# Performance work log

Measured on AMD Instinct MI355X. Metric: run time of the kernel, lower is better.

## Reference

```python
import jax, jax.numpy as jnp
import numpy as np

B, N, E = 4096, 64, 256      # graph pairs, nodes per drug, directed edges per drug
F, H, FP = 128, 64, 2048     # node feat dim, hidden dim, fingerprint dim


def setup_inputs() -> dict:
    key = jax.random.key(0)
    ks = jax.random.split(key, 14)
    return {
        "x1": jax.random.normal(ks[0], (B, N, F), jnp.float32),
        "x2": jax.random.normal(ks[1], (B, N, F), jnp.float32),
        "edge1": jax.random.randint(ks[2], (B, 2, E), 0, N, jnp.int32),
        "edge2": jax.random.randint(ks[3], (B, 2, E), 0, N, jnp.int32),
        "fp1": jax.random.uniform(ks[4], (B, FP), jnp.float32),
        "fp2": jax.random.uniform(ks[5], (B, FP), jnp.float32),
        "W1": jax.random.normal(ks[6], (F, H), jnp.float32) * 0.05,
        "b1": jnp.zeros((H,), jnp.float32),
        "W2": jax.random.normal(ks[7], (H, H), jnp.float32) * 0.05,
        "b2": jnp.zeros((H,), jnp.float32),
        "Wm1": jax.random.normal(ks[8], (2 * H + 2 * FP, 256), jnp.float32) * 0.02,
        "bm1": jnp.zeros((256,), jnp.float32),
        "Wm2": jax.random.normal(ks[9], (256, 1), jnp.float32) * 0.05,
        "bm2": jnp.zeros((1,), jnp.float32),
    }


def gcn_conv(x, src, dst, W, b):
    """PyG GCNConv: self-loops + symmetric normalization, aggregated at dst."""
    n = x.shape[0]
    loops = jnp.arange(n, dtype=src.dtype)
    s = jnp.concatenate([src, loops])
    d = jnp.concatenate([dst, loops])
    deg = jax.ops.segment_sum(jnp.ones_like(d, jnp.float32), d, num_segments=n)
    norm = jax.lax.rsqrt(deg)                      # deg >= 1 due to self-loops
    xw = x @ W                                     # [n, H]
    msg = xw[s] * (norm[s] * norm[d])[:, None]     # [n+E, H]
    return jax.ops.segment_sum(msg, d, num_segments=n) + b


def encode(x, edges, W1, b1, W2, b2):
    src, dst = edges[0], edges[1]
    h = jax.nn.relu(gcn_conv(x, src, dst, W1, b1))
    h = jax.nn.relu(gcn_conv(h, src, dst, W2, b2))
    return h.mean(axis=0)                          # global_mean_pool (1 graph)


_encode_b = jax.vmap(encode, in_axes=(0, 0, None, None, None, None))


def reference(x1, x2, edge1, edge2, fp1, fp2, W1, b1, W2, b2, Wm1, bm1, Wm2, bm2):
    h1 = _encode_b(x1, edge1, W1, b1, W2, b2)      # [B, H]
    h2 = _encode_b(x2, edge2, W1, b1, W2, b2)      # [B, H]
    fused = jnp.concatenate([h1, h2, fp1, fp2], axis=1)  # [B, 2H+2FP]
    hidden = jax.nn.relu(fused @ Wm1 + bm1)
    return jax.nn.sigmoid(hidden @ Wm2 + bm2).reshape(-1)
```

## Files before the change

kernel.cpp:

```cpp
#include <hip/hip_runtime.h>
#include <math.h>

#define B_PAIRS 4096
#define NNODES  64
#define NEDGES  256
#define FDIM    128
#define HDIM    64
#define FPDIM   2048
#define MDIM    256
#define KTOT    4224

typedef __attribute__((ext_vector_type(4))) float f32x4;
typedef __bf16 bf16x8 __attribute__((ext_vector_type(8)));

__device__ __forceinline__ unsigned short f2bf(float f) {
    return __builtin_bit_cast(unsigned short, (__bf16)f);
}
__device__ __forceinline__ unsigned pack2(float a, float b) {
    return (unsigned)f2bf(a) | ((unsigned)f2bf(b) << 16);
}
__device__ __forceinline__ unsigned long long pack4(float a, float b, float c, float d) {
    return (unsigned long long)pack2(a, b) | ((unsigned long long)pack2(c, d) << 32);
}

__global__ void prep_weights(const float* __restrict__ W1, const float* __restrict__ W2,
                             unsigned short* __restrict__ W1t, unsigned short* __restrict__ W2t) {
    const int t0 = blockIdx.x * 256 + threadIdx.x;
    const int stride = gridDim.x * 256;
    for (int i = t0; i < HDIM * FDIM; i += stride) {
        const int n = i >> 7, k = i & 127;
        W1t[i] = f2bf(W1[k * HDIM + n]);
    }
    for (int i = t0; i < HDIM * HDIM; i += stride) {
        const int n = i >> 6, k = i & 63;
        W2t[i] = f2bf(W2[k * HDIM + n]);
    }
}

__global__ __launch_bounds__(256)
void prep_wm1(const float* __restrict__ Wm1, unsigned short* __restrict__ Wm1t) {
    __shared__ float tile[32][33];
    const int k0 = blockIdx.x * 32, n0 = blockIdx.y * 32;
    const int t = threadIdx.x;
    const int c = t & 31, r8 = t >> 5;
    #pragma unroll
    for (int rr = r8; rr < 32; rr += 8)
        tile[rr][c] = Wm1[(size_t)(k0 + rr) * MDIM + n0 + c];
    __syncthreads();
    #pragma unroll
    for (int j = 0; j < 4; ++j) {
        const int n = n0 + r8 + 8 * j;
        Wm1t[(size_t)n * KTOT + k0 + c] = f2bf(tile[c][r8 + 8 * j]);
    }
}

#define WAITLDS() do { __asm__ volatile("s_waitcnt lgkmcnt(0)" ::: "memory"); \
                       __builtin_amdgcn_sched_barrier(0); } while (0)

__global__ __launch_bounds__(64, 2)
void encode_kernel(const float* __restrict__ x1, const float* __restrict__ x2,
                   const int* __restrict__ e1, const int* __restrict__ e2,
                   const unsigned short* __restrict__ W1t, const float* __restrict__ b1,
                   const unsigned short* __restrict__ W2t, const float* __restrict__ b2,
                   float* __restrict__ hbuf) {
    __shared__ __align__(16) unsigned char lds[8960];
    const int gid  = blockIdx.x;
    const int drug = gid >> 12;
    const int b    = gid & (B_PAIRS - 1);
    const float* x  = (drug ? x2 : x1) + (size_t)b * NNODES * FDIM;
    const int*   eg = (drug ? e2 : e1) + (size_t)b * 2 * NEDGES;

    const int t  = threadIdx.x;
    const int lr = t & 15, lg = t >> 4;
    const unsigned swl = (unsigned)(lr & 7) << 4;

    unsigned* cnt = (unsigned*)lds;
    float*    nrm = (float*)(lds + 8448);
    int*      deg = (int*)(lds + 8704);

    float4 xalo[16];
    #pragma unroll
    for (int mt = 0; mt < 2; ++mt) {
        const float* xr = x + (size_t)(16 * mt + lr) * FDIM + 8 * lg;
        #pragma unroll
        for (int ks = 0; ks < 4; ++ks) {
            xalo[mt * 8 + 2 * ks]     = ((const float4*)(xr + 32 * ks))[0];
            xalo[mt * 8 + 2 * ks + 1] = ((const float4*)(xr + 32 * ks))[1];
        }
    }
    const int4 s4 = ((const int4*)eg)[t];
    const int4 d4 = ((const int4*)eg)[t + 64];

    #pragma unroll
    for (int i = 0; i < 8; ++i) ((uint4*)cnt)[t + 64 * i] = make_uint4(0, 0, 0, 0);
    if (t < 16) ((uint4*)cnt)[512 + t] = make_uint4(0, 0, 0, 0);
    deg[t] = 0;
    WAITLDS();

    {
        const int ss[4] = {s4.x, s4.y, s4.z, s4.w};
        const int dd[4] = {d4.x, d4.y, d4.z, d4.w};
        #pragma unroll
        for (int i = 0; i < 4; ++i) {
            atomicAdd(&deg[dd[i]], 1);
            atomicAdd(&cnt[dd[i] * 33 + (ss[i] >> 1)], 1u << ((ss[i] & 1) * 16));
        }
    }
    WAITLDS();

    float4 xahi[16];
    #pragma unroll
    for (int mt = 0; mt < 2; ++mt) {
        const float* xr2 = x + (size_t)(16 * (mt + 2) + lr) * FDIM + 8 * lg;
        #pragma unroll
        for (int ks = 0; ks < 4; ++ks) {
            xahi[mt * 8 + 2 * ks]     = ((const float4*)(xr2 + 32 * ks))[0];
            xahi[mt * 8 + 2 * ks + 1] = ((const float4*)(xr2 + 32 * ks))[1];
        }
    }

    nrm[t] = rsqrtf((float)deg[t] + 1.0f);
    WAITLDS();

    bf16x8 bw1[16];
    #pragma unroll
    for (int nt = 0; nt < 4; ++nt)
        #pragma unroll
        for (int ks = 0; ks < 4; ++ks)
            bw1[nt * 4 + ks] = *(const bf16x8*)(W1t + (16 * nt + lr) * FDIM + 32 * ks + 8 * lg);

    bf16x8 ahat[8];
    {
        const float ncol[2][8] = {
            { nrm[8 * lg + 0], nrm[8 * lg + 1], nrm[8 * lg + 2], nrm[8 * lg + 3],
              nrm[8 * lg + 4], nrm[8 * lg + 5], nrm[8 * lg + 6], nrm[8 * lg + 7] },
            { nrm[32 + 8 * lg + 0], nrm[32 + 8 * lg + 1], nrm[32 + 8 * lg + 2], nrm[32 + 8 * lg + 3],
              nrm[32 + 8 * lg + 4], nrm[32 + 8 * lg + 5], nrm[32 + 8 * lg + 6], nrm[32 + 8 * lg + 7] }
        };
        #pragma unroll
        for (int q = 0; q < 4; ++q) {
            const int r = 16 * q + lr;
            const float nr = nrm[r];
            #pragma unroll
            for (int ks = 0; ks < 2; ++ks) {
                const int c0 = 32 * ks + 8 * lg;
                const uint4 w = *(const uint4*)(cnt + r * 33 + (c0 >> 1));
                const unsigned ww[4] = { w.x, w.y, w.z, w.w };
                bf16x8 f;
                #pragma unroll
                for (int e = 0; e < 8; ++e) {
                    const int c = c0 + e;
                    const unsigned m = (e & 1) ? (ww[e >> 1] >> 16) : (ww[e >> 1] & 0xffffu);
                    const float v = (float)(m + (r == c ? 1u : 0u)) * nr * ncol[ks][e];
                    f[e] = (__bf16)v;
                }
                ahat[q * 2 + ks] = f;
            }
        }
    }
    WAITLDS();

    #pragma unroll
    for (int half = 0; half < 2; ++half) {
        const float4* xs = half ? xahi : xalo;
        #pragma unroll
        for (int m2i = 0; m2i < 2; ++m2i) {
            const int mt = half * 2 + m2i;
            f32x4 acc[4];
            #pragma unroll
            for (int nt = 0; nt < 4; ++nt) acc[nt] = (f32x4){0.f, 0.f, 0.f, 0.f};
            #pragma unroll
            for (int ks = 0; ks < 4; ++ks) {
                bf16x8 a;
                const float4 u = xs[m2i * 8 + 2 * ks], v = xs[m2i * 8 + 2 * ks + 1];
                a[0] = (__bf16)u.x; a[1] = (__bf16)u.y; a[2] = (__bf16)u.z; a[3] = (__bf16)u.w;
                a[4] = (__bf16)v.x; a[5] = (__bf16)v.y; a[6] = (__bf16)v.z; a[7] = (__bf16)v.w;
                #pragma unroll
                for (int nt = 0; nt < 4; ++nt)
                    acc[nt] = __builtin_amdgcn_mfma_f32_16x16x32_bf16(a, bw1[nt * 4 + ks], acc[nt], 0, 0, 0);
            }
            const unsigned m2 = (unsigned)(2 * (16 * mt + 4 * lg));
            #pragma unroll
            for (int nt = 0; nt < 4; ++nt) {
                const int f = 16 * nt + lr;
                *(unsigned long long*)(lds + (unsigned)f * 128 + (m2 ^ swl)) =
                    pack4(acc[nt][0], acc[nt][1], acc[nt][2], acc[nt][3]);
            }
        }
    }
    WAITLDS();

    {
        bf16x8 ta[8];
        #pragma unroll
        for (int mt = 0; mt < 4; ++mt)
            #pragma unroll
            for (int ks = 0; ks < 2; ++ks)
                ta[mt * 2 + ks] = *(const bf16x8*)(lds + (unsigned)(16 * mt + lr) * 128 +
                                                   (((unsigned)(64 * ks + 16 * lg)) ^ swl));
        WAITLDS();
        #pragma unroll
        for (int mt = 0; mt < 4; ++mt) {
            f32x4 acc[4];
            #pragma unroll
            for (int nt = 0; nt < 4; ++nt) acc[nt] = (f32x4){0.f, 0.f, 0.f, 0.f};
            #pragma unroll
            for (int ks = 0; ks < 2; ++ks)
                #pragma unroll
                for (int nt = 0; nt < 4; ++nt)
                    acc[nt] = __builtin_amdgcn_mfma_f32_16x16x32_bf16(ta[mt * 2 + ks], ahat[nt * 2 + ks], acc[nt], 0, 0, 0);
            const int m0 = 16 * mt + 4 * lg;
            const float4 b1v = *(const float4*)(b1 + m0);
            const unsigned m2 = (unsigned)(2 * m0);
            #pragma unroll
            for (int nt = 0; nt < 4; ++nt) {
                const int d = 16 * nt + lr;
                const float v0 = fmaxf(acc[nt][0] + b1v.x, 0.f);
                const float v1 = fmaxf(acc[nt][1] + b1v.y, 0.f);
                const float v2 = fmaxf(acc[nt][2] + b1v.z, 0.f);
                const float v3 = fmaxf(acc[nt][3] + b1v.w, 0.f);
                *(unsigned long long*)(lds + (unsigned)d * 128 + (m2 ^ swl)) =
                    pack4(v0, v1, v2, v3);
            }
        }
    }
    WAITLDS();

    {
        bf16x8 ta[8], bw2[8];
        #pragma unroll
        for (int mt = 0; mt < 4; ++mt)
            #pragma unroll
            for (int ks = 0; ks < 2; ++ks)
                ta[mt * 2 + ks] = *(const bf16x8*)(lds + (unsigned)(16 * mt + lr) * 128 +
                                                   (((unsigned)(64 * ks + 16 * lg)) ^ swl));
        #pragma unroll
        for (int nt = 0; nt < 4; ++nt)
            #pragma unroll
            for (int ks = 0; ks < 2; ++ks)
                bw2[nt * 2 + ks] = *(const bf16x8*)(W2t + (16 * nt + lr) * HDIM + 32 * ks + 8 * lg);
        WAITLDS();
        #pragma unroll
        for (int mt = 0; mt < 4; ++mt) {
            f32x4 acc[4];
            #pragma unroll
            for (int nt = 0; nt < 4; ++nt) acc[nt] = (f32x4){0.f, 0.f, 0.f, 0.f};
            #pragma unroll
            for (int ks = 0; ks < 2; ++ks)
                #pragma unroll
                for (int nt = 0; nt < 4; ++nt)
                    acc[nt] = __builtin_amdgcn_mfma_f32_16x16x32_bf16(ta[mt * 2 + ks], bw2[nt * 2 + ks], acc[nt], 0, 0, 0);
            const unsigned m2 = (unsigned)(2 * (16 * mt + 4 * lg));
            #pragma unroll
            for (int nt = 0; nt < 4; ++nt) {
                const int n = 16 * nt + lr;
                *(unsigned long long*)(lds + (unsigned)n * 128 + (m2 ^ swl)) =
                    pack4(acc[nt][0], acc[nt][1], acc[nt][2], acc[nt][3]);
            }
        }
    }
    WAITLDS();

    {
        bf16x8 bt3[8];
        #pragma unroll
        for (int nt = 0; nt < 4; ++nt)
            #pragma unroll
            for (int ks = 0; ks < 2; ++ks)
                bt3[nt * 2 + ks] = *(const bf16x8*)(lds + (unsigned)(16 * nt + lr) * 128 +
                                                    (((unsigned)(64 * ks + 16 * lg)) ^ swl));
        float b2v[4], p[4];
        #pragma unroll
        for (int nt = 0; nt < 4; ++nt) { b2v[nt] = b2[16 * nt + lr]; p[nt] = 0.f; }
        #pragma unroll
        for (int mt = 0; mt < 4; ++mt) {
            f32x4 acc[4];
            #pragma unroll
            for (int nt = 0; nt < 4; ++nt) acc[nt] = (f32x4){0.f, 0.f, 0.f, 0.f};
            #pragma unroll
            for (int ks = 0; ks < 2; ++ks)
                #pragma unroll
                for (int nt = 0; nt < 4; ++nt)
                    acc[nt] = __builtin_amdgcn_mfma_f32_16x16x32_bf16(ahat[mt * 2 + ks], bt3[nt * 2 + ks], acc[nt], 0, 0, 0);
            #pragma unroll
            for (int nt = 0; nt < 4; ++nt) {
                #pragma unroll
                for (int j = 0; j < 4; ++j) p[nt] += fmaxf(acc[nt][j] + b2v[nt], 0.f);
            }
        }
        #pragma unroll
        for (int nt = 0; nt < 4; ++nt) {
            p[nt] += __shfl_xor(p[nt], 16, 64);
            p[nt] += __shfl_xor(p[nt], 32, 64);
        }
        if (lg == 0) {
            float* hout = hbuf + ((size_t)drug * B_PAIRS + b) * HDIM;
            #pragma unroll
            for (int nt = 0; nt < 4; ++nt) hout[16 * nt + lr] = p[nt] * (1.0f / 64.0f);
        }
    }
}

__global__ __launch_bounds__(256)
void fused_mlp_kernel(const float* __restrict__ fp1, const float* __restrict__ fp2,
                      const float* __restrict__ hbuf,
                      const unsigned short* __restrict__ Wm1t,
                      const float* __restrict__ bm1, const float* __restrict__ Wm2,
                      const float* __restrict__ bm2, float* __restrict__ out) {
    __shared__ __align__(16) unsigned char lds[8448];
    float* pool = (float*)(lds + 8192);
    const int t = threadIdx.x;
    const int lane = t & 63, wid = t >> 6;
    const int lr = lane & 15, lg = lane >> 4;
    const int pair0 = blockIdx.x * 16;

    const int r  = t >> 4;
    const int kc = (t & 15) << 3;
    const int pr = pair0 + r;
    const unsigned wOff = (unsigned)r * 256 + (((unsigned)(2 * kc)) ^ ((unsigned)(r & 7) << 4));

    f32x4 acc[4];
    #pragma unroll
    for (int nf = 0; nf < 4; ++nf) acc[nf] = (f32x4){0.f, 0.f, 0.f, 0.f};

    const unsigned short* brow[4];
    #pragma unroll
    for (int nf = 0; nf < 4; ++nf)
        brow[nf] = Wm1t + (size_t)(64 * wid + 16 * nf + lr) * KTOT + 8 * lg;

    float4 va, vb;
    #define LOAD_A(s)                                                                  \
        {                                                                              \
            const float* src;                                                          \
            if ((s) == 0)                                                              \
                src = (kc < 64) ? hbuf + (size_t)pr * HDIM + kc                        \
                                : hbuf + (size_t)(B_PAIRS + pr) * HDIM + (kc - 64);    \
            else if ((s) <= 16)                                                        \
                src = fp1 + (size_t)pr * FPDIM + ((s) - 1) * 128 + kc;                 \
            else                                                                       \
                src = fp2 + (size_t)pr * FPDIM + ((s) - 17) * 128 + kc;                \
            va = ((const float4*)src)[0];                                              \
            vb = ((const float4*)src)[1];                                              \
        }
    #define STORE_A(base)                                                              \
        *(uint4*)((base) + wOff) = make_uint4(pack2(va.x, va.y), pack2(va.z, va.w),    \
                                              pack2(vb.x, vb.y), pack2(vb.z, vb.w));

    LOAD_A(0);
    STORE_A(lds);
    for (int s = 0; s < 33; ++s) {
        const bool more = (s + 1 < 33);
        if (more) LOAD_A(s + 1);
        __syncthreads();
        const unsigned char* buf = lds + (unsigned)((s & 1) << 12);
        const unsigned asw = (unsigned)(lr & 7) << 4;
        const int kglob = s << 7;
        #pragma unroll
        for (int ks = 0; ks < 4; ++ks) {
            const unsigned kb = (unsigned)(64 * ks + 16 * lg);
            const bf16x8 a = *(const bf16x8*)(buf + (unsigned)lr * 256 + (kb ^ asw));
            #pragma unroll
            for (int nf = 0; nf < 4; ++nf) {
                const bf16x8 bw = *(const bf16x8*)(brow[nf] + kglob + 32 * ks);
                acc[nf] = __builtin_amdgcn_mfma_f32_16x16x32_bf16(a, bw, acc[nf], 0, 0, 0);
            }
        }
        if (more) STORE_A(lds + (unsigned)(((s + 1) & 1) << 12));
    }

    float bm1v[4], wm2v[4];
    #pragma unroll
    for (int nf = 0; nf < 4; ++nf) {
        const int n = 64 * wid + 16 * nf + lr;
        bm1v[nf] = bm1[n];
        wm2v[nf] = Wm2[n];
    }
    #pragma unroll
    for (int reg = 0; reg < 4; ++reg) {
        float p = 0.f;
        #pragma unroll
        for (int nf = 0; nf < 4; ++nf)
            p += fmaxf(acc[nf][reg] + bm1v[nf], 0.f) * wm2v[nf];
        p += __shfl_xor(p, 1, 64);
        p += __shfl_xor(p, 2, 64);
        p += __shfl_xor(p, 4, 64);
        p += __shfl_xor(p, 8, 64);
        if (lr == 0) pool[wid * 16 + 4 * lg + reg] = p;
    }
    __syncthreads();
    if (t < 16) {
        const float y = pool[t] + pool[16 + t] + pool[32 + t] + pool[48 + t] + bm2[0];
        out[pair0 + t] = 1.0f / (1.0f + expf(-y));
    }
    #undef LOAD_A
    #undef STORE_A
}

extern "C" void kernel_launch(void* const* d_in, const int* in_sizes, int n_in,
                              void* d_out, int out_size, void* d_ws, size_t ws_size,
                              hipStream_t stream) {
    const float* x1  = (const float*)d_in[0];
    const float* x2  = (const float*)d_in[1];
    const int*   e1  = (const int*)d_in[2];
    const int*   e2  = (const int*)d_in[3];
    const float* fp1 = (const float*)d_in[4];
    const float* fp2 = (const float*)d_in[5];
    const float* W1  = (const float*)d_in[6];
    const float* b1  = (const float*)d_in[7];
    const float* W2  = (const float*)d_in[8];
    const float* b2  = (const float*)d_in[9];
    const float* Wm1 = (const float*)d_in[10];
    const float* bm1 = (const float*)d_in[11];
    const float* Wm2 = (const float*)d_in[12];
    const float* bm2 = (const float*)d_in[13];
    float* out  = (float*)d_out;

    float* hbuf = (float*)d_ws;
    unsigned short* W1t  = (unsigned short*)((char*)d_ws + (2 << 20));
    unsigned short* W2t  = W1t + HDIM * FDIM;
    unsigned short* Wm1t = (unsigned short*)((char*)d_ws + (3 << 20));

    hipLaunchKernelGGL(prep_weights, dim3(16), dim3(256), 0, stream, W1, W2, W1t, W2t);
    hipLaunchKernelGGL(prep_wm1, dim3(132, 8), dim3(256), 0, stream, Wm1, Wm1t);
    hipLaunchKernelGGL(encode_kernel, dim3(2 * B_PAIRS), dim3(64), 0, stream,
                       x1, x2, e1, e2, W1t, b1, W2t, b2, hbuf);
    hipLaunchKernelGGL(fused_mlp_kernel, dim3(B_PAIRS / 16), dim3(256), 0, stream,
                       fp1, fp2, hbuf, Wm1t, bm1, Wm2, bm2, out);
}
```

Baseline: 160.8 us.

## Pack four graph encodes per block and derive degrees from count matrix

```diff
diff --git a/kernel.cpp b/kernel.cpp
--- a/kernel.cpp
+++ b/kernel.cpp
@@ -9,6 +9,7 @@
 #define FPDIM   2048
 #define MDIM    256
 #define KTOT    4224
+#define SLICE   8704
 
 typedef __attribute__((ext_vector_type(4))) float f32x4;
 typedef __bf16 bf16x8 __attribute__((ext_vector_type(8)));
@@ -57,26 +58,27 @@
 #define WAITLDS() do { __asm__ volatile("s_waitcnt lgkmcnt(0)" ::: "memory"); \
                        __builtin_amdgcn_sched_barrier(0); } while (0)
 
-__global__ __launch_bounds__(64, 2)
+__global__ __launch_bounds__(256, 4)
 void encode_kernel(const float* __restrict__ x1, const float* __restrict__ x2,
                    const int* __restrict__ e1, const int* __restrict__ e2,
                    const unsigned short* __restrict__ W1t, const float* __restrict__ b1,
                    const unsigned short* __restrict__ W2t, const float* __restrict__ b2,
                    float* __restrict__ hbuf) {
-    __shared__ __align__(16) unsigned char lds[8960];
-    const int gid  = blockIdx.x;
+    __shared__ __align__(16) unsigned char lds[4 * SLICE];
+    const int wid = threadIdx.x >> 6;
+    const int t   = threadIdx.x & 63;
+    const int gid  = blockIdx.x * 4 + wid;
     const int drug = gid >> 12;
     const int b    = gid & (B_PAIRS - 1);
     const float* x  = (drug ? x2 : x1) + (size_t)b * NNODES * FDIM;
     const int*   eg = (drug ? e2 : e1) + (size_t)b * 2 * NEDGES;
 
-    const int t  = threadIdx.x;
     const int lr = t & 15, lg = t >> 4;
     const unsigned swl = (unsigned)(lr & 7) << 4;
 
-    unsigned* cnt = (unsigned*)lds;
-    float*    nrm = (float*)(lds + 8448);
-    int*      deg = (int*)(lds + 8704);
+    unsigned char* sl = lds + wid * SLICE;
+    unsigned* cnt = (unsigned*)sl;
+    float*    nrm = (float*)(sl + 8448);
 
     float4 xalo[16];
     #pragma unroll
@@ -93,18 +95,15 @@
 
     #pragma unroll
     for (int i = 0; i < 8; ++i) ((uint4*)cnt)[t + 64 * i] = make_uint4(0, 0, 0, 0);
-    if (t < 16) ((uint4*)cnt)[512 + t] = make_uint4(0, 0, 0, 0);
-    deg[t] = 0;
+    cnt[2048 + t] = 0;
     WAITLDS();
 
     {
         const int ss[4] = {s4.x, s4.y, s4.z, s4.w};
         const int dd[4] = {d4.x, d4.y, d4.z, d4.w};
         #pragma unroll
-        for (int i = 0; i < 4; ++i) {
-            atomicAdd(&deg[dd[i]], 1);
+        for (int i = 0; i < 4; ++i)
             atomicAdd(&cnt[dd[i] * 33 + (ss[i] >> 1)], 1u << ((ss[i] & 1) * 16));
-        }
     }
     WAITLDS();
 
@@ -119,7 +118,15 @@
         }
     }
 
-    nrm[t] = rsqrtf((float)deg[t] + 1.0f);
+    {
+        unsigned ssum = 0;
+        #pragma unroll
+        for (int j = 0; j < 33; ++j) {
+            const unsigned w = cnt[t * 33 + j];
+            ssum += (w & 0xffffu) + (w >> 16);
+        }
+        nrm[t] = rsqrtf((float)ssum + 1.0f);
+    }
     WAITLDS();
 
     bf16x8 bw1[16];
@@ -183,7 +190,7 @@
             #pragma unroll
             for (int nt = 0; nt < 4; ++nt) {
                 const int f = 16 * nt + lr;
-                *(unsigned long long*)(lds + (unsigned)f * 128 + (m2 ^ swl)) =
+                *(unsigned long long*)(sl + (unsigned)f * 128 + (m2 ^ swl)) =
                     pack4(acc[nt][0], acc[nt][1], acc[nt][2], acc[nt][3]);
             }
         }
@@ -196,7 +203,7 @@
         for (int mt = 0; mt < 4; ++mt)
             #pragma unroll
             for (int ks = 0; ks < 2; ++ks)
-                ta[mt * 2 + ks] = *(const bf16x8*)(lds + (unsigned)(16 * mt + lr) * 128 +
+                ta[mt * 2 + ks] = *(const bf16x8*)(sl + (unsigned)(16 * mt + lr) * 128 +
                                                    (((unsigned)(64 * ks + 16 * lg)) ^ swl));
         WAITLDS();
         #pragma unroll
@@ -219,7 +226,7 @@
                 const float v1 = fmaxf(acc[nt][1] + b1v.y, 0.f);
                 const float v2 = fmaxf(acc[nt][2] + b1v.z, 0.f);
                 const float v3 = fmaxf(acc[nt][3] + b1v.w, 0.f);
-                *(unsigned long long*)(lds + (unsigned)d * 128 + (m2 ^ swl)) =
+                *(unsigned long long*)(sl + (unsigned)d * 128 + (m2 ^ swl)) =
                     pack4(v0, v1, v2, v3);
             }
         }
@@ -232,7 +239,7 @@
         for (int mt = 0; mt < 4; ++mt)
             #pragma unroll
             for (int ks = 0; ks < 2; ++ks)
-                ta[mt * 2 + ks] = *(const bf16x8*)(lds + (unsigned)(16 * mt + lr) * 128 +
+                ta[mt * 2 + ks] = *(const bf16x8*)(sl + (unsigned)(16 * mt + lr) * 128 +
                                                    (((unsigned)(64 * ks + 16 * lg)) ^ swl));
         #pragma unroll
         for (int nt = 0; nt < 4; ++nt)
@@ -254,7 +261,7 @@
             #pragma unroll
             for (int nt = 0; nt < 4; ++nt) {
                 const int n = 16 * nt + lr;
-                *(unsigned long long*)(lds + (unsigned)n * 128 + (m2 ^ swl)) =
+                *(unsigned long long*)(sl + (unsigned)n * 128 + (m2 ^ swl)) =
                     pack4(acc[nt][0], acc[nt][1], acc[nt][2], acc[nt][3]);
             }
         }
@@ -267,7 +274,7 @@
         for (int nt = 0; nt < 4; ++nt)
             #pragma unroll
             for (int ks = 0; ks < 2; ++ks)
-                bt3[nt * 2 + ks] = *(const bf16x8*)(lds + (unsigned)(16 * nt + lr) * 128 +
+                bt3[nt * 2 + ks] = *(const bf16x8*)(sl + (unsigned)(16 * nt + lr) * 128 +
                                                     (((unsigned)(64 * ks + 16 * lg)) ^ swl));
         float b2v[4], p[4];
         #pragma unroll
@@ -422,7 +429,7 @@
 
     hipLaunchKernelGGL(prep_weights, dim3(16), dim3(256), 0, stream, W1, W2, W1t, W2t);
     hipLaunchKernelGGL(prep_wm1, dim3(132, 8), dim3(256), 0, stream, Wm1, Wm1t);
-    hipLaunchKernelGGL(encode_kernel, dim3(2 * B_PAIRS), dim3(64), 0, stream,
+    hipLaunchKernelGGL(encode_kernel, dim3(2 * B_PAIRS / 4), dim3(256), 0, stream,
                        x1, x2, e1, e2, W1t, b1, W2t, b2, hbuf);
     hipLaunchKernelGGL(fused_mlp_kernel, dim3(B_PAIRS / 16), dim3(256), 0, stream,
                        fp1, fp2, hbuf, Wm1t, bm1, Wm2, bm2, out);
```

Result: slower. 236.6 us (+47.2%).

## Split MLP hidden dimension across two blocks and combine partial sums

Applied to the files above, without the earlier changes.

```diff
diff --git a/kernel.cpp b/kernel.cpp
--- a/kernel.cpp
+++ b/kernel.cpp
@@ -302,31 +302,32 @@
 }
 
 __global__ __launch_bounds__(256)
-void fused_mlp_kernel(const float* __restrict__ fp1, const float* __restrict__ fp2,
-                      const float* __restrict__ hbuf,
-                      const unsigned short* __restrict__ Wm1t,
-                      const float* __restrict__ bm1, const float* __restrict__ Wm2,
-                      const float* __restrict__ bm2, float* __restrict__ out) {
+void mlp_half_kernel(const float* __restrict__ fp1, const float* __restrict__ fp2,
+                     const float* __restrict__ hbuf,
+                     const unsigned short* __restrict__ Wm1t,
+                     const float* __restrict__ bm1, const float* __restrict__ Wm2,
+                     float* __restrict__ P) {
     __shared__ __align__(16) unsigned char lds[8448];
     float* pool = (float*)(lds + 8192);
     const int t = threadIdx.x;
     const int lane = t & 63, wid = t >> 6;
     const int lr = lane & 15, lg = lane >> 4;
     const int pair0 = blockIdx.x * 16;
+    const int ns = blockIdx.y;
 
     const int r  = t >> 4;
     const int kc = (t & 15) << 3;
     const int pr = pair0 + r;
     const unsigned wOff = (unsigned)r * 256 + (((unsigned)(2 * kc)) ^ ((unsigned)(r & 7) << 4));
 
-    f32x4 acc[4];
-    #pragma unroll
-    for (int nf = 0; nf < 4; ++nf) acc[nf] = (f32x4){0.f, 0.f, 0.f, 0.f};
-
-    const unsigned short* brow[4];
-    #pragma unroll
-    for (int nf = 0; nf < 4; ++nf)
-        brow[nf] = Wm1t + (size_t)(64 * wid + 16 * nf + lr) * KTOT + 8 * lg;
+    f32x4 acc[2];
+    acc[0] = (f32x4){0.f, 0.f, 0.f, 0.f};
+    acc[1] = (f32x4){0.f, 0.f, 0.f, 0.f};
+
+    const unsigned short* brow[2];
+    #pragma unroll
+    for (int nf = 0; nf < 2; ++nf)
+        brow[nf] = Wm1t + (size_t)(128 * ns + 32 * wid + 16 * nf + lr) * KTOT + 8 * lg;
 
     float4 va, vb;
     #define LOAD_A(s)                                                                  \
@@ -360,7 +361,7 @@
             const unsigned kb = (unsigned)(64 * ks + 16 * lg);
             const bf16x8 a = *(const bf16x8*)(buf + (unsigned)lr * 256 + (kb ^ asw));
             #pragma unroll
-            for (int nf = 0; nf < 4; ++nf) {
+            for (int nf = 0; nf < 2; ++nf) {
                 const bf16x8 bw = *(const bf16x8*)(brow[nf] + kglob + 32 * ks);
                 acc[nf] = __builtin_amdgcn_mfma_f32_16x16x32_bf16(a, bw, acc[nf], 0, 0, 0);
             }
@@ -368,10 +369,10 @@
         if (more) STORE_A(lds + (unsigned)(((s + 1) & 1) << 12));
     }
 
-    float bm1v[4], wm2v[4];
-    #pragma unroll
-    for (int nf = 0; nf < 4; ++nf) {
-        const int n = 64 * wid + 16 * nf + lr;
+    float bm1v[2], wm2v[2];
+    #pragma unroll
+    for (int nf = 0; nf < 2; ++nf) {
+        const int n = 128 * ns + 32 * wid + 16 * nf + lr;
         bm1v[nf] = bm1[n];
         wm2v[nf] = Wm2[n];
     }
@@ -379,7 +380,7 @@
     for (int reg = 0; reg < 4; ++reg) {
         float p = 0.f;
         #pragma unroll
-        for (int nf = 0; nf < 4; ++nf)
+        for (int nf = 0; nf < 2; ++nf)
             p += fmaxf(acc[nf][reg] + bm1v[nf], 0.f) * wm2v[nf];
         p += __shfl_xor(p, 1, 64);
         p += __shfl_xor(p, 2, 64);
@@ -388,12 +389,18 @@
         if (lr == 0) pool[wid * 16 + 4 * lg + reg] = p;
     }
     __syncthreads();
-    if (t < 16) {
-        const float y = pool[t] + pool[16 + t] + pool[32 + t] + pool[48 + t] + bm2[0];
-        out[pair0 + t] = 1.0f / (1.0f + expf(-y));
-    }
+    if (t < 16)
+        P[(size_t)ns * B_PAIRS + pair0 + t] = pool[t] + pool[16 + t] + pool[32 + t] + pool[48 + t];
     #undef LOAD_A
     #undef STORE_A
+}
+
+__global__ __launch_bounds__(256)
+void combine_kernel(const float* __restrict__ P, const float* __restrict__ bm2,
+                    float* __restrict__ out) {
+    const int i = blockIdx.x * 256 + threadIdx.x;
+    const float y = P[i] + P[B_PAIRS + i] + bm2[0];
+    out[i] = 1.0f / (1.0f + expf(-y));
 }
 
 extern "C" void kernel_launch(void* const* d_in, const int* in_sizes, int n_in,
@@ -419,11 +426,14 @@
     unsigned short* W1t  = (unsigned short*)((char*)d_ws + (2 << 20));
     unsigned short* W2t  = W1t + HDIM * FDIM;
     unsigned short* Wm1t = (unsigned short*)((char*)d_ws + (3 << 20));
+    float* P = (float*)((char*)d_ws + (6 << 20));
 
     hipLaunchKernelGGL(prep_weights, dim3(16), dim3(256), 0, stream, W1, W2, W1t, W2t);
     hipLaunchKernelGGL(prep_wm1, dim3(132, 8), dim3(256), 0, stream, Wm1, Wm1t);
     hipLaunchKernelGGL(encode_kernel, dim3(2 * B_PAIRS), dim3(64), 0, stream,
                        x1, x2, e1, e2, W1t, b1, W2t, b2, hbuf);
-    hipLaunchKernelGGL(fused_mlp_kernel, dim3(B_PAIRS / 16), dim3(256), 0, stream,
-                       fp1, fp2, hbuf, Wm1t, bm1, Wm2, bm2, out);
-}
+    hipLaunchKernelGGL(mlp_half_kernel, dim3(B_PAIRS / 16, 2), dim3(256), 0, stream,
+                       fp1, fp2, hbuf, Wm1t, bm1, Wm2, P);
+    hipLaunchKernelGGL(combine_kernel, dim3(B_PAIRS / 256), dim3(256), 0, stream,
+                       P, bm2, out);
+}
```

After: 172.1 us. 7.0% more time.
